# Kernel tuning notes

Measured on AMD Instinct MI355X. Metric: run time of the kernel, lower is better.

## Reference

```python
import jax, jax.numpy as jnp
import numpy as np

N_POI = 50000
D = 128
E = 400000
GCN_NUM = 3
HEADS = 8
B = 64
L = 100
LEAKY_SLOPE = 0.01
NORM_EPS = 1e-12


def setup_inputs() -> dict:
    key = jax.random.key(0)
    ks = jax.random.split(key, 11)
    return {
        "embeds": jax.random.normal(ks[0], (N_POI, D), jnp.float32) * 0.1,
        "gcn_W": jax.random.normal(ks[1], (GCN_NUM, D, D), jnp.float32) * (1.0 / np.sqrt(D)),
        "gcn_b": jnp.zeros((GCN_NUM, D), jnp.float32),
        "in_proj_w": jax.random.normal(ks[2], (3 * D, D), jnp.float32) * (1.0 / np.sqrt(D)),
        "in_proj_b": jnp.zeros((3 * D,), jnp.float32),
        "out_proj_w": jax.random.normal(ks[3], (D, D), jnp.float32) * (1.0 / np.sqrt(D)),
        "out_proj_b": jnp.zeros((D,), jnp.float32),
        "dist_vec": jax.random.uniform(ks[4], (E,), jnp.float32),
        "dist_edges": jax.random.randint(ks[5], (2, E), 0, N_POI),
        "x_idx": jax.random.randint(ks[6], (B * L,), 0, N_POI),
        "poi_idx": jax.random.randint(ks[7], (B,), 0, N_POI),
    }


def _self_attn(x, in_w, in_b, out_w, out_b):
    # x: [B, L, D]; standard nn.MultiheadAttention with Q=K=V=x, batch_first
    b, l, d = x.shape
    hd = d // HEADS
    qkv = x @ in_w.T + in_b                      # [B, L, 3D]
    q, k, v = jnp.split(qkv, 3, axis=-1)
    def heads(t):
        return t.reshape(b, l, HEADS, hd).transpose(0, 2, 1, 3)  # [B, H, L, hd]
    q, k, v = heads(q), heads(k), heads(v)
    scores = jnp.einsum('bhqd,bhkd->bhqk', q, k) / jnp.sqrt(jnp.asarray(hd, x.dtype))
    attn = jax.nn.softmax(scores, axis=-1)
    o = jnp.einsum('bhqk,bhkd->bhqd', attn, v).transpose(0, 2, 1, 3).reshape(b, l, d)
    return o @ out_w.T + out_b


def reference(embeds, gcn_W, gcn_b, in_proj_w, in_proj_b, out_proj_w, out_proj_b,
              dist_vec, dist_edges, x_idx, poi_idx):
    n_poi = embeds.shape[0]
    loop = jnp.arange(n_poi)
    # symmetrize edges + add self-loops (done in GeoGraph.__init__)
    rows = jnp.concatenate([dist_edges[0], dist_edges[1], loop])
    cols = jnp.concatenate([dist_edges[1], dist_edges[0], loop])
    dv = jnp.concatenate([dist_vec, dist_vec, jnp.zeros((n_poi,), dist_vec.dtype)])
    # symmetric degree normalization over destination (col) index
    deg = jax.ops.segment_sum(jnp.ones_like(dv), cols, num_segments=n_poi)
    dis = jnp.where(deg > 0, jax.lax.rsqrt(jnp.maximum(deg, 1e-12)), 0.0)
    w = jnp.exp(-dv ** 2) * dis[rows] * dis[cols]   # [E_full]

    enc = embeds
    for i in range(GCN_NUM):
        # sparse.mm: out[row] += w * enc[col]
        agg = jax.ops.segment_sum(w[:, None] * enc[cols], rows, num_segments=n_poi)
        enc = agg @ gcn_W[i].T + gcn_b[i]
        enc = jax.nn.leaky_relu(enc, LEAKY_SLOPE)
        enc = enc / jnp.maximum(jnp.linalg.norm(enc, axis=-1, keepdims=True), NORM_EPS)

    tar_embed = enc[poi_idx]                         # [B, D]
    geo_feat = enc[x_idx].reshape(B, L, D)           # equal-length sessions -> pad is a reshape
    attn_out = _self_attn(geo_feat, in_proj_w, in_proj_b, out_proj_w, out_proj_b)
    aggr_feat = attn_out.mean(axis=1)                # [B, D]
    return aggr_feat, tar_embed
```

## Files before the change

kernel.cpp:

```cpp
#include <hip/hip_runtime.h>
#include <math.h>

#define D 128
#define GCN_NUM 3
#define HEADS 8
#define HD 16
#define L_SEQ 100
#define LEAKY 0.01f
#define SC_BUCKETS 8

typedef __attribute__((ext_vector_type(8))) short short8v;
typedef __attribute__((ext_vector_type(4))) float f32x4;

__device__ __forceinline__ unsigned f2bf(float x) {
  unsigned u = __float_as_uint(x);
  return (u + 0x7FFFu + ((u >> 16) & 1u)) >> 16;
}
__device__ __forceinline__ float bflo2f(unsigned u) { return __uint_as_float(u << 16); }
__device__ __forceinline__ float bfhi2f(unsigned u) { return __uint_as_float(u & 0xFFFF0000u); }


__global__ void prep(const float* __restrict__ s0, unsigned short* __restrict__ d0, int n0,
                     const float* __restrict__ s1, unsigned short* __restrict__ d1, int n1,
                     const float* __restrict__ s2, unsigned short* __restrict__ d2, int n2,
                     int* __restrict__ deg, int N) {
  int i = blockIdx.x * blockDim.x + threadIdx.x;
  int n4tot = n0 + n1 + n2;
  if (i < n4tot) {
    const float* s; unsigned short* d; int j;
    if (i < n0)           { s = s0; d = d0; j = i; }
    else if (i < n0 + n1) { s = s1; d = d1; j = i - n0; }
    else                  { s = s2; d = d2; j = i - n0 - n1; }
    float4 v = reinterpret_cast<const float4*>(s)[j];
    uint2 o;
    o.x = f2bf(v.x) | (f2bf(v.y) << 16);
    o.y = f2bf(v.z) | (f2bf(v.w) << 16);
    reinterpret_cast<uint2*>(d)[j] = o;
  } else if (i - n4tot < N) {
    deg[i - n4tot] = 1;
  }
}


__global__ void count_deg(const int* __restrict__ e0, const int* __restrict__ e1,
                          int* __restrict__ deg, int E) {
  int stride = gridDim.x * blockDim.x;
  for (int i = blockIdx.x * blockDim.x + threadIdx.x; i < E; i += stride) {
    atomicAdd(&deg[e0[i]], 1);
    atomicAdd(&deg[e1[i]], 1);
  }
}


__global__ __launch_bounds__(1024) void block_sum(const int* __restrict__ deg,
                                                  int* __restrict__ bsum, int n) {
  __shared__ int ws[16];
  int tid = threadIdx.x, lane = tid & 63, wid = tid >> 6;
  int i = blockIdx.x * 1024 + tid;
  int v = (i < n) ? deg[i] : 0;
#pragma unroll
  for (int off = 32; off; off >>= 1) v += __shfl_xor(v, off);
  if (lane == 0) ws[wid] = v;
  __syncthreads();
  if (tid == 0) {
    int s = 0;
#pragma unroll
    for (int k = 0; k < 16; ++k) s += ws[k];
    bsum[blockIdx.x] = s;
  }
}

__global__ __launch_bounds__(1024) void scan_final(
    const int* __restrict__ deg, const int* __restrict__ bsum,
    int* __restrict__ row_ptr, int* __restrict__ cursor, int n, int nb) {
  __shared__ int ws[16];
  __shared__ int prefix_s;
  int tid = threadIdx.x, lane = tid & 63, wid = tid >> 6;
  int i = blockIdx.x * 1024 + tid;
  int v = (i < n) ? deg[i] : 0;
  int x = v;
#pragma unroll
  for (int off = 1; off < 64; off <<= 1) {
    int y = __shfl_up(x, off);
    if (lane >= off) x += y;
  }
  if (lane == 63) ws[wid] = x;
  __syncthreads();
  if (wid == 0) {
    int pv = (lane < blockIdx.x) ? bsum[lane] : 0;
#pragma unroll
    for (int off = 32; off; off >>= 1) pv += __shfl_xor(pv, off);
    if (lane == 0) prefix_s = pv;
    int s = (lane < 16) ? ws[lane] : 0;
#pragma unroll
    for (int off = 1; off < 16; off <<= 1) {
      int y = __shfl_up(s, off);
      if (lane >= off) s += y;
    }
    if (lane < 16) ws[lane] = s;
  }
  __syncthreads();
  int woff = wid ? ws[wid - 1] : 0;
  int prefix = prefix_s;
  if (i < n) {
    int pval = prefix + woff + (x - v);
    row_ptr[i] = pval;
    cursor[i] = pval;
  }
  if (blockIdx.x == nb - 1 && tid == 0) row_ptr[n] = prefix + ws[15];
}

__global__ __launch_bounds__(256) void scatter_edges_x(
    const int* __restrict__ e0, const int* __restrict__ e1,
    const float* __restrict__ dv, const int* __restrict__ deg,
    int* __restrict__ cursor, uint2* __restrict__ ecw,
    int E, int N, int span, int bpb) {
  int bucket = blockIdx.x & (SC_BUCKETS - 1);
  int bx = blockIdx.x >> 3;
  int rlo = bucket * span;
  int rhi = min(rlo + span, N);
  int total = 2 * E + N;
  int stride = bpb * 256;
  for (int i = bx * 256 + threadIdx.x; i < total; i += stride) {
    int r, c; bool self = false;
    if (i < E)          { r = e0[i];     c = e1[i]; }
    else if (i < 2 * E) { r = e1[i - E]; c = e0[i - E]; }
    else                { r = i - 2 * E; c = r; self = true; }
    if (r < rlo || r >= rhi) continue;
    float d = self ? 0.f : dv[(i < E) ? i : i - E];
    float w = expf(-d * d) * (1.0f / sqrtf((float)deg[r])) * (1.0f / sqrtf((float)deg[c]));
    int pos = atomicAdd(&cursor[r], 1);
    ecw[pos] = make_uint2((unsigned)c, __float_as_uint(w));
  }
}


__global__ __launch_bounds__(256) void spmm_bf(
    const int* __restrict__ row_ptr, const uint2* __restrict__ ecw,
    const unsigned short* __restrict__ enc, unsigned short* __restrict__ agg, int n) {
  int r = blockIdx.x * 4 + (threadIdx.x >> 6);
  if (r >= n) return;
  int lane = threadIdx.x & 63;
  int g = lane >> 4, t = lane & 15;
  int s = row_ptr[r], e = row_ptr[r + 1];
  float a0 = 0.f, a1 = 0.f, a2 = 0.f, a3 = 0.f, a4 = 0.f, a5 = 0.f, a6 = 0.f, a7 = 0.f;
  int i = s + g;
  uint2 cwA = make_uint2(0u, 0u), cwB = make_uint2(0u, 0u);
  if (i < e) cwA = ecw[i];
  if (i + 4 < e) cwB = ecw[i + 4];
  while (i + 4 < e) {
    uint2 cwC = cwA, cwD = cwB;
    if (i + 8 < e)  cwC = ecw[i + 8];
    if (i + 12 < e) cwD = ecw[i + 12];
    float wA = __uint_as_float(cwA.y), wB = __uint_as_float(cwB.y);
    uint4 uA = *reinterpret_cast<const uint4*>(enc + (size_t)cwA.x * D + t * 8);
    uint4 uB = *reinterpret_cast<const uint4*>(enc + (size_t)cwB.x * D + t * 8);
    a0 = fmaf(wA, bflo2f(uA.x), a0); a1 = fmaf(wA, bfhi2f(uA.x), a1);
    a2 = fmaf(wA, bflo2f(uA.y), a2); a3 = fmaf(wA, bfhi2f(uA.y), a3);
    a4 = fmaf(wA, bflo2f(uA.z), a4); a5 = fmaf(wA, bfhi2f(uA.z), a5);
    a6 = fmaf(wA, bflo2f(uA.w), a6); a7 = fmaf(wA, bfhi2f(uA.w), a7);
    a0 = fmaf(wB, bflo2f(uB.x), a0); a1 = fmaf(wB, bfhi2f(uB.x), a1);
    a2 = fmaf(wB, bflo2f(uB.y), a2); a3 = fmaf(wB, bfhi2f(uB.y), a3);
    a4 = fmaf(wB, bflo2f(uB.z), a4); a5 = fmaf(wB, bfhi2f(uB.z), a5);
    a6 = fmaf(wB, bflo2f(uB.w), a6); a7 = fmaf(wB, bfhi2f(uB.w), a7);
    cwA = cwC; cwB = cwD;
    i += 8;
  }
  if (i < e) {
    float wA = __uint_as_float(cwA.y);
    uint4 uA = *reinterpret_cast<const uint4*>(enc + (size_t)cwA.x * D + t * 8);
    a0 = fmaf(wA, bflo2f(uA.x), a0); a1 = fmaf(wA, bfhi2f(uA.x), a1);
    a2 = fmaf(wA, bflo2f(uA.y), a2); a3 = fmaf(wA, bfhi2f(uA.y), a3);
    a4 = fmaf(wA, bflo2f(uA.z), a4); a5 = fmaf(wA, bfhi2f(uA.z), a5);
    a6 = fmaf(wA, bflo2f(uA.w), a6); a7 = fmaf(wA, bfhi2f(uA.w), a7);
  }
  a0 += __shfl_xor(a0, 16); a0 += __shfl_xor(a0, 32);
  a1 += __shfl_xor(a1, 16); a1 += __shfl_xor(a1, 32);
  a2 += __shfl_xor(a2, 16); a2 += __shfl_xor(a2, 32);
  a3 += __shfl_xor(a3, 16); a3 += __shfl_xor(a3, 32);
  a4 += __shfl_xor(a4, 16); a4 += __shfl_xor(a4, 32);
  a5 += __shfl_xor(a5, 16); a5 += __shfl_xor(a5, 32);
  a6 += __shfl_xor(a6, 16); a6 += __shfl_xor(a6, 32);
  a7 += __shfl_xor(a7, 16); a7 += __shfl_xor(a7, 32);
  if (g == 0) {
    uint4 o;
    o.x = f2bf(a0) | (f2bf(a1) << 16);
    o.y = f2bf(a2) | (f2bf(a3) << 16);
    o.z = f2bf(a4) | (f2bf(a5) << 16);
    o.w = f2bf(a6) | (f2bf(a7) << 16);
    *reinterpret_cast<uint4*>(agg + (size_t)r * D + t * 8) = o;
  }
}

__global__ __launch_bounds__(256) void dense_mfma(
    const unsigned short* __restrict__ A, const unsigned short* __restrict__ Wb,
    const float* __restrict__ bias, unsigned short* __restrict__ enc, int n) {
  __shared__ unsigned short Wl[128 * 136];
  int tid = threadIdx.x;
  {
    int cg = (tid & 15) * 8;
    int r0 = tid >> 4;
#pragma unroll
    for (int i = 0; i < 8; ++i) {
      int row = r0 + i * 16;
      *reinterpret_cast<short8v*>(&Wl[row * 136 + cg]) =
          *reinterpret_cast<const short8v*>(Wb + row * D + cg);
    }
  }
  __syncthreads();
  int w = tid >> 6, lane = tid & 63;
  int lr = lane & 15, lg = lane >> 4;
#pragma unroll
  for (int rt = 0; rt < 2; ++rt) {
    int rbase = blockIdx.x * 128 + rt * 64 + w * 16;
    f32x4 acc[8];
#pragma unroll
    for (int j = 0; j < 8; ++j) acc[j] = f32x4{0.f, 0.f, 0.f, 0.f};
    const unsigned short* arow = A + (size_t)(rbase + lr) * D + lg * 8;
#pragma unroll
    for (int ks = 0; ks < 4; ++ks) {
      short8v a = *reinterpret_cast<const short8v*>(arow + ks * 32);
#pragma unroll
      for (int jt = 0; jt < 8; ++jt) {
        short8v b = *reinterpret_cast<const short8v*>(&Wl[(jt * 16 + lr) * 136 + ks * 32 + lg * 8]);
        acc[jt] = __builtin_amdgcn_mfma_f32_16x16x32_bf16(a, b, acc[jt], 0, 0, 0);
      }
    }
    float vals[8][4];
    float ss[4] = {0.f, 0.f, 0.f, 0.f};
#pragma unroll
    for (int jt = 0; jt < 8; ++jt) {
      float bj = bias[jt * 16 + lr];
#pragma unroll
      for (int i = 0; i < 4; ++i) {
        float t = acc[jt][i] + bj;
        t = (t > 0.f) ? t : LEAKY * t;
        vals[jt][i] = t;
        ss[i] += t * t;
      }
    }
#pragma unroll
    for (int i = 0; i < 4; ++i) {
      float s = ss[i];
      s += __shfl_xor(s, 1); s += __shfl_xor(s, 2);
      s += __shfl_xor(s, 4); s += __shfl_xor(s, 8);
      ss[i] = 1.0f / fmaxf(sqrtf(s), 1e-12f);
    }
#pragma unroll
    for (int i = 0; i < 4; ++i) {
      int row = rbase + lg * 4 + i;
      if (row < n) {
#pragma unroll
        for (int jt = 0; jt < 8; ++jt)
          enc[(size_t)row * D + jt * 16 + lr] = (unsigned short)f2bf(vals[jt][i] * ss[i]);
      }
    }
  }
}


__global__ void gather_tar(const unsigned short* __restrict__ src,
                           const int* __restrict__ poi_idx, float* __restrict__ tar, int B) {
  int j = blockIdx.x;
  if (j < B) {
    int t = threadIdx.x;
    unsigned u = reinterpret_cast<const unsigned*>(src + (size_t)poi_idx[j] * D)[t];
    reinterpret_cast<float2*>(tar + (size_t)j * D)[t] = make_float2(bflo2f(u), bfhi2f(u));
  }
}

__global__ __launch_bounds__(256) void qkv_mfma(
    const unsigned short* __restrict__ enc, const int* __restrict__ x_idx,
    const unsigned short* __restrict__ Wb, const float* __restrict__ bias,
    float* __restrict__ qkv, int M) {
  __shared__ unsigned short Wl[128 * 136];
  int tid = threadIdx.x;
  const unsigned short* Wslab = Wb + (size_t)blockIdx.y * 128 * D;
  {
    int cg = (tid & 15) * 8;
    int r0 = tid >> 4;
#pragma unroll
    for (int i = 0; i < 8; ++i) {
      int row = r0 + i * 16;
      *reinterpret_cast<short8v*>(&Wl[row * 136 + cg]) =
          *reinterpret_cast<const short8v*>(Wslab + row * D + cg);
    }
  }
  __syncthreads();
  int w = tid >> 6, lane = tid & 63;
  int lr = lane & 15, lg = lane >> 4;
  int colbase = blockIdx.y * 128;
#pragma unroll
  for (int rt = 0; rt < 2; ++rt) {
    int rbase = blockIdx.x * 128 + rt * 64 + w * 16;
    f32x4 acc[8];
#pragma unroll
    for (int j = 0; j < 8; ++j) acc[j] = f32x4{0.f, 0.f, 0.f, 0.f};
    const unsigned short* arow = enc + (size_t)x_idx[rbase + lr] * D + lg * 8;
#pragma unroll
    for (int ks = 0; ks < 4; ++ks) {
      short8v a = *reinterpret_cast<const short8v*>(arow + ks * 32);
#pragma unroll
      for (int jt = 0; jt < 8; ++jt) {
        short8v b = *reinterpret_cast<const short8v*>(&Wl[(jt * 16 + lr) * 136 + ks * 32 + lg * 8]);
        acc[jt] = __builtin_amdgcn_mfma_f32_16x16x32_bf16(a, b, acc[jt], 0, 0, 0);
      }
    }
#pragma unroll
    for (int jt = 0; jt < 8; ++jt) {
      int j = colbase + jt * 16 + lr;
      float bj = bias[j];
#pragma unroll
      for (int i = 0; i < 4; ++i) {
        int row = rbase + lg * 4 + i;
        if (row < M) qkv[(size_t)row * 384 + j] = acc[jt][i] + bj;
      }
    }
  }
}

__global__ __launch_bounds__(128) void attn_kernel(
    const float* __restrict__ qkv, float* __restrict__ o) {
  __shared__ float k_s[L_SEQ][HD];
  __shared__ float v_s[L_SEQ][HD];
  __shared__ float sc[L_SEQ][L_SEQ + 1];
  int b = blockIdx.x / HEADS;
  int h = blockIdx.x % HEADS;
  int tid = threadIdx.x;
  const size_t rowbase = (size_t)b * L_SEQ;
  for (int idx = tid; idx < L_SEQ * HD; idx += 128) {
    int l = idx >> 4, d2 = idx & 15;
    const float* base = qkv + (rowbase + l) * 384 + h * HD + d2;
    k_s[l][d2] = base[128];
    v_s[l][d2] = base[256];
  }
  __syncthreads();
  if (tid < L_SEQ) {
    float q[HD];
    const float* qp = qkv + (rowbase + tid) * 384 + h * HD;
#pragma unroll
    for (int d2 = 0; d2 < HD; ++d2) q[d2] = qp[d2];
    float m = -1e30f;
    for (int j = 0; j < L_SEQ; ++j) {
      float s = 0.f;
#pragma unroll
      for (int d2 = 0; d2 < HD; ++d2) s += q[d2] * k_s[j][d2];
      s *= 0.25f;
      sc[tid][j] = s;
      m = fmaxf(m, s);
    }
    float sum = 0.f;
    for (int j = 0; j < L_SEQ; ++j) {
      float e = expf(sc[tid][j] - m);
      sc[tid][j] = e;
      sum += e;
    }
    float inv = 1.f / sum;
    float oacc[HD];
#pragma unroll
    for (int d2 = 0; d2 < HD; ++d2) oacc[d2] = 0.f;
    for (int j = 0; j < L_SEQ; ++j) {
      float p = sc[tid][j];
#pragma unroll
      for (int d2 = 0; d2 < HD; ++d2) oacc[d2] += p * v_s[j][d2];
    }
    float* op = o + (rowbase + tid) * D + h * HD;
#pragma unroll
    for (int d2 = 0; d2 < HD; ++d2) op[d2] = oacc[d2] * inv;
  }
}

__global__ __launch_bounds__(128) void out_mean_kernel(
    const float* __restrict__ o, const float* __restrict__ Wo,
    const float* __restrict__ bo, float* __restrict__ out, int L) {
  __shared__ float m_s[D];
  int b = blockIdx.x, tid = threadIdx.x;
  float s = 0.f;
  for (int l = 0; l < L; ++l) s += o[((size_t)b * L + l) * D + tid];
  m_s[tid] = s / (float)L;
  __syncthreads();
  const float4* w4 = reinterpret_cast<const float4*>(Wo + (size_t)tid * D);
  float acc = 0.f;
  for (int k4 = 0; k4 < D / 4; ++k4) {
    float4 w = w4[k4];
    int k = k4 * 4;
    acc += m_s[k] * w.x + m_s[k + 1] * w.y + m_s[k + 2] * w.z + m_s[k + 3] * w.w;
  }
  out[(size_t)b * D + tid] = acc + bo[tid];
}


extern "C" void kernel_launch(void* const* d_in, const int* in_sizes, int n_in,
                              void* d_out, int out_size, void* d_ws, size_t ws_size,
                              hipStream_t stream) {
  const float* embeds   = (const float*)d_in[0];
  const float* gcn_W    = (const float*)d_in[1];
  const float* gcn_b    = (const float*)d_in[2];
  const float* in_w     = (const float*)d_in[3];
  const float* in_b     = (const float*)d_in[4];
  const float* out_w    = (const float*)d_in[5];
  const float* out_b    = (const float*)d_in[6];
  const float* dist_vec = (const float*)d_in[7];
  const int*   edges    = (const int*)d_in[8];
  const int*   x_idx    = (const int*)d_in[9];
  const int*   poi_idx  = (const int*)d_in[10];
  float* out = (float*)d_out;

  int N  = in_sizes[0] / D;
  int E  = in_sizes[7];
  int BL = in_sizes[9];
  int B  = in_sizes[10];
  int L  = BL / B;
  const int* e0 = edges;
  const int* e1 = edges + E;
  size_t total_edges = (size_t)2 * E + N;
  int Npad = ((N + 127) / 128) * 128;
  int NB   = (N + 1023) / 1024;

  char* p = (char*)d_ws;
  auto alloc = [&](size_t bytes) { char* q = p; p += (bytes + 255) & ~(size_t)255; return q; };
  int*   deg     = (int*)alloc((size_t)N * 4);
  int*   row_ptr = (int*)alloc((size_t)(N + 1) * 4);
  int*   cursor  = (int*)alloc((size_t)N * 4);
  int*   bsum    = (int*)alloc((size_t)NB * 4);
  uint2* ecw     = (uint2*)alloc(total_edges * 8);
  unsigned short* emb_bf = (unsigned short*)alloc((size_t)Npad * D * 2);
  unsigned short* W_bf   = (unsigned short*)alloc((size_t)GCN_NUM * D * D * 2);
  unsigned short* inw_bf = (unsigned short*)alloc((size_t)3 * D * D * 2);
  unsigned short* agg_bf = (unsigned short*)alloc((size_t)Npad * D * 2);
  unsigned short* enc_bf = (unsigned short*)alloc((size_t)Npad * D * 2);
  float* qkv  = (float*)alloc((size_t)BL * 384 * 4);
  float* obuf = (float*)alloc((size_t)BL * D * 4);

  int n4e = N * D / 4, n4w = GCN_NUM * D * D / 4, n4i = 3 * D * D / 4;
  int prep_tot = n4e + n4w + n4i + N;
  prep<<<(prep_tot + 255) / 256, 256, 0, stream>>>(
      embeds, emb_bf, n4e, gcn_W, W_bf, n4w, in_w, inw_bf, n4i, deg, N);

  count_deg<<<1024, 256, 0, stream>>>(e0, e1, deg, E);
  block_sum<<<NB, 1024, 0, stream>>>(deg, bsum, N);
  scan_final<<<NB, 1024, 0, stream>>>(deg, bsum, row_ptr, cursor, N, NB);
  int span = (N + SC_BUCKETS - 1) / SC_BUCKETS;
  int bpb = 512;
  scatter_edges_x<<<SC_BUCKETS * bpb, 256, 0, stream>>>(
      e0, e1, dist_vec, deg, cursor, ecw, E, N, span, bpb);

  const unsigned short* cur_in = emb_bf;
  for (int i = 0; i < GCN_NUM; ++i) {
    spmm_bf<<<(N + 3) / 4, 256, 0, stream>>>(row_ptr, ecw, cur_in, agg_bf, N);
    dense_mfma<<<Npad / 128, 256, 0, stream>>>(
        agg_bf, W_bf + (size_t)i * D * D, gcn_b + (size_t)i * D, enc_bf, N);
    cur_in = enc_bf;
  }

  gather_tar<<<B, 64, 0, stream>>>(enc_bf, poi_idx, out + (size_t)B * D, B);
  dim3 qgrid(BL / 128, 3);
  qkv_mfma<<<qgrid, 256, 0, stream>>>(enc_bf, x_idx, inw_bf, in_b, qkv, BL);
  attn_kernel<<<B * HEADS, 128, 0, stream>>>(qkv, obuf);
  out_mean_kernel<<<B, 128, 0, stream>>>(obuf, out_w, out_b, out, L);
}
```

Baseline: 364.4 us.

## Bucket edge scatter by hardware XCC id with per-bucket dynamic chunk queue

The edge scatter kernel now reads the hardware XCC id and assigns each block to the row bucket of the chiplet it runs on. Blocks then pull edge chunks from a per-bucket atomic work counter, which prep resets to zero. The aim is to keep each bucket's cursor atomics and ecw writes local to one XCC's L2 and to balance work dynamically. It assumes blocks are spread over all 8 XCCs; if any XCC runs no blocks, that bucket's edges are never written. It also adds a global atomic and two barriers per chunk.

```diff
diff --git a/kernel.cpp b/kernel.cpp
--- a/kernel.cpp
+++ b/kernel.cpp
@@ -8,6 +8,7 @@
 #define L_SEQ 100
 #define LEAKY 0.01f
 #define SC_BUCKETS 8
+#define SC_CHUNK 2048
 
 typedef __attribute__((ext_vector_type(8))) short short8v;
 typedef __attribute__((ext_vector_type(4))) float f32x4;
@@ -23,7 +24,7 @@
 __global__ void prep(const float* __restrict__ s0, unsigned short* __restrict__ d0, int n0,
                      const float* __restrict__ s1, unsigned short* __restrict__ d1, int n1,
                      const float* __restrict__ s2, unsigned short* __restrict__ d2, int n2,
-                     int* __restrict__ deg, int N) {
+                     int* __restrict__ deg, int N, int* __restrict__ chunk_ctr) {
   int i = blockIdx.x * blockDim.x + threadIdx.x;
   int n4tot = n0 + n1 + n2;
   if (i < n4tot) {
@@ -39,6 +40,7 @@
   } else if (i - n4tot < N) {
     deg[i - n4tot] = 1;
   }
+  if (i < SC_BUCKETS) chunk_ctr[i] = 0;
 }
 
 
@@ -110,27 +112,38 @@
   if (blockIdx.x == nb - 1 && tid == 0) row_ptr[n] = prefix + ws[15];
 }
 
-__global__ __launch_bounds__(256) void scatter_edges_x(
+__global__ __launch_bounds__(256) void scatter_edges_xcc(
     const int* __restrict__ e0, const int* __restrict__ e1,
     const float* __restrict__ dv, const int* __restrict__ deg,
-    int* __restrict__ cursor, uint2* __restrict__ ecw,
-    int E, int N, int span, int bpb) {
-  int bucket = blockIdx.x & (SC_BUCKETS - 1);
-  int bx = blockIdx.x >> 3;
+    int* __restrict__ cursor, int* __restrict__ chunk_ctr, uint2* __restrict__ ecw,
+    int E, int N, int span) {
+  unsigned xcc;
+  asm volatile("s_getreg_b32 %0, hwreg(HW_REG_XCC_ID)" : "=s"(xcc));
+  int bucket = (int)(xcc & (SC_BUCKETS - 1));
   int rlo = bucket * span;
   int rhi = min(rlo + span, N);
   int total = 2 * E + N;
-  int stride = bpb * 256;
-  for (int i = bx * 256 + threadIdx.x; i < total; i += stride) {
-    int r, c; bool self = false;
-    if (i < E)          { r = e0[i];     c = e1[i]; }
-    else if (i < 2 * E) { r = e1[i - E]; c = e0[i - E]; }
-    else                { r = i - 2 * E; c = r; self = true; }
-    if (r < rlo || r >= rhi) continue;
-    float d = self ? 0.f : dv[(i < E) ? i : i - E];
-    float w = expf(-d * d) * (1.0f / sqrtf((float)deg[r])) * (1.0f / sqrtf((float)deg[c]));
-    int pos = atomicAdd(&cursor[r], 1);
-    ecw[pos] = make_uint2((unsigned)c, __float_as_uint(w));
+  int nchunks = (total + SC_CHUNK - 1) / SC_CHUNK;
+  __shared__ int chunk_s;
+  for (;;) {
+    __syncthreads();
+    if (threadIdx.x == 0) chunk_s = atomicAdd(&chunk_ctr[bucket], 1);
+    __syncthreads();
+    int ch = chunk_s;
+    if (ch >= nchunks) break;
+    int base = ch * SC_CHUNK;
+    int end = min(base + SC_CHUNK, total);
+    for (int i = base + (int)threadIdx.x; i < end; i += 256) {
+      int r, c; bool self = false;
+      if (i < E)          { r = e0[i];     c = e1[i]; }
+      else if (i < 2 * E) { r = e1[i - E]; c = e0[i - E]; }
+      else                { r = i - 2 * E; c = r; self = true; }
+      if (r < rlo || r >= rhi) continue;
+      float d = self ? 0.f : dv[(i < E) ? i : i - E];
+      float w = expf(-d * d) * (1.0f / sqrtf((float)deg[r])) * (1.0f / sqrtf((float)deg[c]));
+      int pos = atomicAdd(&cursor[r], 1);
+      ecw[pos] = make_uint2((unsigned)c, __float_as_uint(w));
+    }
   }
 }
 
@@ -419,11 +432,12 @@
 
   char* p = (char*)d_ws;
   auto alloc = [&](size_t bytes) { char* q = p; p += (bytes + 255) & ~(size_t)255; return q; };
-  int*   deg     = (int*)alloc((size_t)N * 4);
-  int*   row_ptr = (int*)alloc((size_t)(N + 1) * 4);
-  int*   cursor  = (int*)alloc((size_t)N * 4);
-  int*   bsum    = (int*)alloc((size_t)NB * 4);
-  uint2* ecw     = (uint2*)alloc(total_edges * 8);
+  int*   deg       = (int*)alloc((size_t)N * 4);
+  int*   row_ptr   = (int*)alloc((size_t)(N + 1) * 4);
+  int*   cursor    = (int*)alloc((size_t)N * 4);
+  int*   bsum      = (int*)alloc((size_t)NB * 4);
+  int*   chunk_ctr = (int*)alloc((size_t)SC_BUCKETS * 4);
+  uint2* ecw       = (uint2*)alloc(total_edges * 8);
   unsigned short* emb_bf = (unsigned short*)alloc((size_t)Npad * D * 2);
   unsigned short* W_bf   = (unsigned short*)alloc((size_t)GCN_NUM * D * D * 2);
   unsigned short* inw_bf = (unsigned short*)alloc((size_t)3 * D * D * 2);
@@ -435,15 +449,14 @@
   int n4e = N * D / 4, n4w = GCN_NUM * D * D / 4, n4i = 3 * D * D / 4;
   int prep_tot = n4e + n4w + n4i + N;
   prep<<<(prep_tot + 255) / 256, 256, 0, stream>>>(
-      embeds, emb_bf, n4e, gcn_W, W_bf, n4w, in_w, inw_bf, n4i, deg, N);
+      embeds, emb_bf, n4e, gcn_W, W_bf, n4w, in_w, inw_bf, n4i, deg, N, chunk_ctr);
 
   count_deg<<<1024, 256, 0, stream>>>(e0, e1, deg, E);
   block_sum<<<NB, 1024, 0, stream>>>(deg, bsum, N);
   scan_final<<<NB, 1024, 0, stream>>>(deg, bsum, row_ptr, cursor, N, NB);
   int span = (N + SC_BUCKETS - 1) / SC_BUCKETS;
-  int bpb = 512;
-  scatter_edges_x<<<SC_BUCKETS * bpb, 256, 0, stream>>>(
-      e0, e1, dist_vec, deg, cursor, ecw, E, N, span, bpb);
+  scatter_edges_xcc<<<2048, 256, 0, stream>>>(
+      e0, e1, dist_vec, deg, cursor, chunk_ctr, ecw, E, N, span);
 
   const unsigned short* cur_in = emb_bf;
   for (int i = 0; i < GCN_NUM; ++i) {
```

After: 408.7 us. 1.12x slower.

## Slice features per XCD and pack edges into 32-bit col/bf16 weight

Applied to the files above, without the earlier changes.

Stores node embeddings in 8 feature slices of 16 columns each. The new SpMM reads the hardware XCC id so that each XCD processes only one slice, keeping that slice's gather working set inside its own L2. Row chunks are handed out dynamically through per-slice atomic counters, which are reset in the prep kernel. Each edge is packed into 32 bits (16-bit column index plus bf16 weight), halving edge traffic. The catches are that node counts must stay below 65536, edge weights lose precision, and the dense and gather kernels must read and write the strided slice layout.

```diff
diff --git a/kernel.cpp b/kernel.cpp
--- a/kernel.cpp
+++ b/kernel.cpp
@@ -23,14 +23,22 @@
 __global__ void prep(const float* __restrict__ s0, unsigned short* __restrict__ d0, int n0,
                      const float* __restrict__ s1, unsigned short* __restrict__ d1, int n1,
                      const float* __restrict__ s2, unsigned short* __restrict__ d2, int n2,
-                     int* __restrict__ deg, int N) {
+                     int* __restrict__ deg, int N, int* __restrict__ ctr, size_t strideS) {
   int i = blockIdx.x * blockDim.x + threadIdx.x;
   int n4tot = n0 + n1 + n2;
-  if (i < n4tot) {
+  if (i < n0) {
+    float4 v = reinterpret_cast<const float4*>(s0)[i];
+    int row = i >> 5;
+    int k = (i & 31) * 4;
+    uint2 o;
+    o.x = f2bf(v.x) | (f2bf(v.y) << 16);
+    o.y = f2bf(v.z) | (f2bf(v.w) << 16);
+    unsigned short* dst = d0 + (size_t)(k >> 4) * strideS + (size_t)row * 16 + (k & 15);
+    *reinterpret_cast<uint2*>(dst) = o;
+  } else if (i < n4tot) {
     const float* s; unsigned short* d; int j;
-    if (i < n0)           { s = s0; d = d0; j = i; }
-    else if (i < n0 + n1) { s = s1; d = d1; j = i - n0; }
-    else                  { s = s2; d = d2; j = i - n0 - n1; }
+    if (i < n0 + n1) { s = s1; d = d1; j = i - n0; }
+    else             { s = s2; d = d2; j = i - n0 - n1; }
     float4 v = reinterpret_cast<const float4*>(s)[j];
     uint2 o;
     o.x = f2bf(v.x) | (f2bf(v.y) << 16);
@@ -39,6 +47,7 @@
   } else if (i - n4tot < N) {
     deg[i - n4tot] = 1;
   }
+  if (i < GCN_NUM * 8) ctr[i] = 0;
 }
 
 
@@ -50,7 +59,6 @@
     atomicAdd(&deg[e1[i]], 1);
   }
 }
-
 
 __global__ __launch_bounds__(1024) void block_sum(const int* __restrict__ deg,
                                                   int* __restrict__ bsum, int n) {
@@ -110,10 +118,10 @@
   if (blockIdx.x == nb - 1 && tid == 0) row_ptr[n] = prefix + ws[15];
 }
 
-__global__ __launch_bounds__(256) void scatter_edges_x(
+__global__ __launch_bounds__(256) void scatter_edges_p(
     const int* __restrict__ e0, const int* __restrict__ e1,
     const float* __restrict__ dv, const int* __restrict__ deg,
-    int* __restrict__ cursor, uint2* __restrict__ ecw,
+    int* __restrict__ cursor, unsigned* __restrict__ ecw,
     int E, int N, int span, int bpb) {
   int bucket = blockIdx.x & (SC_BUCKETS - 1);
   int bx = blockIdx.x >> 3;
@@ -130,71 +138,64 @@
     float d = self ? 0.f : dv[(i < E) ? i : i - E];
     float w = expf(-d * d) * (1.0f / sqrtf((float)deg[r])) * (1.0f / sqrtf((float)deg[c]));
     int pos = atomicAdd(&cursor[r], 1);
-    ecw[pos] = make_uint2((unsigned)c, __float_as_uint(w));
-  }
-}
-
-
-__global__ __launch_bounds__(256) void spmm_bf(
-    const int* __restrict__ row_ptr, const uint2* __restrict__ ecw,
-    const unsigned short* __restrict__ enc, unsigned short* __restrict__ agg, int n) {
-  int r = blockIdx.x * 4 + (threadIdx.x >> 6);
-  if (r >= n) return;
-  int lane = threadIdx.x & 63;
-  int g = lane >> 4, t = lane & 15;
-  int s = row_ptr[r], e = row_ptr[r + 1];
-  float a0 = 0.f, a1 = 0.f, a2 = 0.f, a3 = 0.f, a4 = 0.f, a5 = 0.f, a6 = 0.f, a7 = 0.f;
-  int i = s + g;
-  uint2 cwA = make_uint2(0u, 0u), cwB = make_uint2(0u, 0u);
-  if (i < e) cwA = ecw[i];
-  if (i + 4 < e) cwB = ecw[i + 4];
-  while (i + 4 < e) {
-    uint2 cwC = cwA, cwD = cwB;
-    if (i + 8 < e)  cwC = ecw[i + 8];
-    if (i + 12 < e) cwD = ecw[i + 12];
-    float wA = __uint_as_float(cwA.y), wB = __uint_as_float(cwB.y);
-    uint4 uA = *reinterpret_cast<const uint4*>(enc + (size_t)cwA.x * D + t * 8);
-    uint4 uB = *reinterpret_cast<const uint4*>(enc + (size_t)cwB.x * D + t * 8);
-    a0 = fmaf(wA, bflo2f(uA.x), a0); a1 = fmaf(wA, bfhi2f(uA.x), a1);
-    a2 = fmaf(wA, bflo2f(uA.y), a2); a3 = fmaf(wA, bfhi2f(uA.y), a3);
-    a4 = fmaf(wA, bflo2f(uA.z), a4); a5 = fmaf(wA, bfhi2f(uA.z), a5);
-    a6 = fmaf(wA, bflo2f(uA.w), a6); a7 = fmaf(wA, bfhi2f(uA.w), a7);
-    a0 = fmaf(wB, bflo2f(uB.x), a0); a1 = fmaf(wB, bfhi2f(uB.x), a1);
-    a2 = fmaf(wB, bflo2f(uB.y), a2); a3 = fmaf(wB, bfhi2f(uB.y), a3);
-    a4 = fmaf(wB, bflo2f(uB.z), a4); a5 = fmaf(wB, bfhi2f(uB.z), a5);
-    a6 = fmaf(wB, bflo2f(uB.w), a6); a7 = fmaf(wB, bfhi2f(uB.w), a7);
-    cwA = cwC; cwB = cwD;
-    i += 8;
-  }
-  if (i < e) {
-    float wA = __uint_as_float(cwA.y);
-    uint4 uA = *reinterpret_cast<const uint4*>(enc + (size_t)cwA.x * D + t * 8);
-    a0 = fmaf(wA, bflo2f(uA.x), a0); a1 = fmaf(wA, bfhi2f(uA.x), a1);
-    a2 = fmaf(wA, bflo2f(uA.y), a2); a3 = fmaf(wA, bfhi2f(uA.y), a3);
-    a4 = fmaf(wA, bflo2f(uA.z), a4); a5 = fmaf(wA, bfhi2f(uA.z), a5);
-    a6 = fmaf(wA, bflo2f(uA.w), a6); a7 = fmaf(wA, bfhi2f(uA.w), a7);
-  }
-  a0 += __shfl_xor(a0, 16); a0 += __shfl_xor(a0, 32);
-  a1 += __shfl_xor(a1, 16); a1 += __shfl_xor(a1, 32);
-  a2 += __shfl_xor(a2, 16); a2 += __shfl_xor(a2, 32);
-  a3 += __shfl_xor(a3, 16); a3 += __shfl_xor(a3, 32);
-  a4 += __shfl_xor(a4, 16); a4 += __shfl_xor(a4, 32);
-  a5 += __shfl_xor(a5, 16); a5 += __shfl_xor(a5, 32);
-  a6 += __shfl_xor(a6, 16); a6 += __shfl_xor(a6, 32);
-  a7 += __shfl_xor(a7, 16); a7 += __shfl_xor(a7, 32);
-  if (g == 0) {
-    uint4 o;
-    o.x = f2bf(a0) | (f2bf(a1) << 16);
-    o.y = f2bf(a2) | (f2bf(a3) << 16);
-    o.z = f2bf(a4) | (f2bf(a5) << 16);
-    o.w = f2bf(a6) | (f2bf(a7) << 16);
-    *reinterpret_cast<uint4*>(agg + (size_t)r * D + t * 8) = o;
+    ecw[pos] = (unsigned)c | (f2bf(w) << 16);
+  }
+}
+
+
+__global__ __launch_bounds__(256) void spmm_slice(
+    const int* __restrict__ row_ptr, const unsigned* __restrict__ ecw,
+    const unsigned short* __restrict__ in_s, unsigned short* __restrict__ out_s,
+    int* __restrict__ ctr, int n, size_t strideS) {
+  unsigned xcc;
+  asm volatile("s_getreg_b32 %0, hwreg(HW_REG_XCC_ID)" : "=s"(xcc));
+  int slice = (int)(xcc & 7u);
+  const unsigned short* in = in_s + (size_t)slice * strideS;
+  unsigned short* out = out_s + (size_t)slice * strideS;
+  int tid = threadIdx.x;
+  int grp = tid >> 4;
+  int sub = (tid >> 3) & 1;
+  int fl = tid & 7;
+  int nch = (n + 63) >> 6;
+  __shared__ int chunk_s;
+  for (;;) {
+    __syncthreads();
+    if (tid == 0) chunk_s = atomicAdd(&ctr[slice], 1);
+    __syncthreads();
+    int ch = chunk_s;
+    if (ch >= nch) break;
+    int rbase = ch << 6;
+#pragma unroll
+    for (int ps = 0; ps < 4; ++ps) {
+      int r = rbase + ps * 16 + grp;
+      if (r >= n) continue;
+      int sE = row_ptr[r], eE = row_ptr[r + 1];
+      float acc0 = 0.f, acc1 = 0.f;
+      int i = sE + sub;
+      unsigned dA = (i < eE) ? ecw[i] : 0u;
+      unsigned dB = (i + 2 < eE) ? ecw[i + 2] : 0u;
+      while (i < eE) {
+        unsigned dn = (i + 4 < eE) ? ecw[i + 4] : 0u;
+        float w = bfhi2f(dA);
+        unsigned u = *reinterpret_cast<const unsigned*>(in + (size_t)(dA & 0xFFFFu) * 16 + fl * 2);
+        acc0 = fmaf(w, bflo2f(u), acc0);
+        acc1 = fmaf(w, bfhi2f(u), acc1);
+        dA = dB; dB = dn; i += 2;
+      }
+      acc0 += __shfl_xor(acc0, 8);
+      acc1 += __shfl_xor(acc1, 8);
+      if (sub == 0) {
+        unsigned o = f2bf(acc0) | (f2bf(acc1) << 16);
+        *reinterpret_cast<unsigned*>(out + (size_t)r * 16 + fl * 2) = o;
+      }
+    }
   }
 }
 
 __global__ __launch_bounds__(256) void dense_mfma(
     const unsigned short* __restrict__ A, const unsigned short* __restrict__ Wb,
-    const float* __restrict__ bias, unsigned short* __restrict__ enc, int n) {
+    const float* __restrict__ bias, unsigned short* __restrict__ enc,
+    int n, size_t strideS) {
   __shared__ unsigned short Wl[128 * 136];
   int tid = threadIdx.x;
   {
@@ -216,10 +217,10 @@
     f32x4 acc[8];
 #pragma unroll
     for (int j = 0; j < 8; ++j) acc[j] = f32x4{0.f, 0.f, 0.f, 0.f};
-    const unsigned short* arow = A + (size_t)(rbase + lr) * D + lg * 8;
+    const unsigned short* abase = A + (size_t)(rbase + lr) * 16 + (lg & 1) * 8;
 #pragma unroll
     for (int ks = 0; ks < 4; ++ks) {
-      short8v a = *reinterpret_cast<const short8v*>(arow + ks * 32);
+      short8v a = *reinterpret_cast<const short8v*>(abase + (size_t)(2 * ks + (lg >> 1)) * strideS);
 #pragma unroll
       for (int jt = 0; jt < 8; ++jt) {
         short8v b = *reinterpret_cast<const short8v*>(&Wl[(jt * 16 + lr) * 136 + ks * 32 + lg * 8]);
@@ -252,7 +253,8 @@
       if (row < n) {
 #pragma unroll
         for (int jt = 0; jt < 8; ++jt)
-          enc[(size_t)row * D + jt * 16 + lr] = (unsigned short)f2bf(vals[jt][i] * ss[i]);
+          enc[(size_t)jt * strideS + (size_t)row * 16 + lr] =
+              (unsigned short)f2bf(vals[jt][i] * ss[i]);
       }
     }
   }
@@ -260,11 +262,15 @@
 
 
 __global__ void gather_tar(const unsigned short* __restrict__ src,
-                           const int* __restrict__ poi_idx, float* __restrict__ tar, int B) {
+                           const int* __restrict__ poi_idx, float* __restrict__ tar,
+                           int B, size_t strideS) {
   int j = blockIdx.x;
   if (j < B) {
     int t = threadIdx.x;
-    unsigned u = reinterpret_cast<const unsigned*>(src + (size_t)poi_idx[j] * D)[t];
+    int f = t * 2;
+    size_t idx = (size_t)poi_idx[j];
+    unsigned u = *reinterpret_cast<const unsigned*>(
+        src + (size_t)(f >> 4) * strideS + idx * 16 + (f & 15));
     reinterpret_cast<float2*>(tar + (size_t)j * D)[t] = make_float2(bflo2f(u), bfhi2f(u));
   }
 }
@@ -272,7 +278,7 @@
 __global__ __launch_bounds__(256) void qkv_mfma(
     const unsigned short* __restrict__ enc, const int* __restrict__ x_idx,
     const unsigned short* __restrict__ Wb, const float* __restrict__ bias,
-    float* __restrict__ qkv, int M) {
+    float* __restrict__ qkv, int M, size_t strideS) {
   __shared__ unsigned short Wl[128 * 136];
   int tid = threadIdx.x;
   const unsigned short* Wslab = Wb + (size_t)blockIdx.y * 128 * D;
@@ -296,10 +302,11 @@
     f32x4 acc[8];
 #pragma unroll
     for (int j = 0; j < 8; ++j) acc[j] = f32x4{0.f, 0.f, 0.f, 0.f};
-    const unsigned short* arow = enc + (size_t)x_idx[rbase + lr] * D + lg * 8;
+    const unsigned short* abase =
+        enc + (size_t)x_idx[rbase + lr] * 16 + (lg & 1) * 8;
 #pragma unroll
     for (int ks = 0; ks < 4; ++ks) {
-      short8v a = *reinterpret_cast<const short8v*>(arow + ks * 32);
+      short8v a = *reinterpret_cast<const short8v*>(abase + (size_t)(2 * ks + (lg >> 1)) * strideS);
 #pragma unroll
       for (int jt = 0; jt < 8; ++jt) {
         short8v b = *reinterpret_cast<const short8v*>(&Wl[(jt * 16 + lr) * 136 + ks * 32 + lg * 8]);
@@ -416,14 +423,16 @@
   size_t total_edges = (size_t)2 * E + N;
   int Npad = ((N + 127) / 128) * 128;
   int NB   = (N + 1023) / 1024;
+  size_t strideS = (size_t)Npad * 16;
 
   char* p = (char*)d_ws;
   auto alloc = [&](size_t bytes) { char* q = p; p += (bytes + 255) & ~(size_t)255; return q; };
-  int*   deg     = (int*)alloc((size_t)N * 4);
-  int*   row_ptr = (int*)alloc((size_t)(N + 1) * 4);
-  int*   cursor  = (int*)alloc((size_t)N * 4);
-  int*   bsum    = (int*)alloc((size_t)NB * 4);
-  uint2* ecw     = (uint2*)alloc(total_edges * 8);
+  int*      deg      = (int*)alloc((size_t)N * 4);
+  int*      row_ptr  = (int*)alloc((size_t)(N + 1) * 4);
+  int*      cursor   = (int*)alloc((size_t)N * 4);
+  int*      bsum     = (int*)alloc((size_t)NB * 4);
+  int*      spmm_ctr = (int*)alloc((size_t)GCN_NUM * 8 * 4);
+  unsigned* ecw      = (unsigned*)alloc(total_edges * 4);
   unsigned short* emb_bf = (unsigned short*)alloc((size_t)Npad * D * 2);
   unsigned short* W_bf   = (unsigned short*)alloc((size_t)GCN_NUM * D * D * 2);
   unsigned short* inw_bf = (unsigned short*)alloc((size_t)3 * D * D * 2);
@@ -435,27 +444,28 @@
   int n4e = N * D / 4, n4w = GCN_NUM * D * D / 4, n4i = 3 * D * D / 4;
   int prep_tot = n4e + n4w + n4i + N;
   prep<<<(prep_tot + 255) / 256, 256, 0, stream>>>(
-      embeds, emb_bf, n4e, gcn_W, W_bf, n4w, in_w, inw_bf, n4i, deg, N);
+      embeds, emb_bf, n4e, gcn_W, W_bf, n4w, in_w, inw_bf, n4i, deg, N, spmm_ctr, strideS);
 
   count_deg<<<1024, 256, 0, stream>>>(e0, e1, deg, E);
   block_sum<<<NB, 1024, 0, stream>>>(deg, bsum, N);
   scan_final<<<NB, 1024, 0, stream>>>(deg, bsum, row_ptr, cursor, N, NB);
   int span = (N + SC_BUCKETS - 1) / SC_BUCKETS;
   int bpb = 512;
-  scatter_edges_x<<<SC_BUCKETS * bpb, 256, 0, stream>>>(
+  scatter_edges_p<<<SC_BUCKETS * bpb, 256, 0, stream>>>(
       e0, e1, dist_vec, deg, cursor, ecw, E, N, span, bpb);
 
   const unsigned short* cur_in = emb_bf;
   for (int i = 0; i < GCN_NUM; ++i) {
-    spmm_bf<<<(N + 3) / 4, 256, 0, stream>>>(row_ptr, ecw, cur_in, agg_bf, N);
+    spmm_slice<<<2048, 256, 0, stream>>>(row_ptr, ecw, cur_in, agg_bf,
+                                         spmm_ctr + i * 8, N, strideS);
     dense_mfma<<<Npad / 128, 256, 0, stream>>>(
-        agg_bf, W_bf + (size_t)i * D * D, gcn_b + (size_t)i * D, enc_bf, N);
+        agg_bf, W_bf + (size_t)i * D * D, gcn_b + (size_t)i * D, enc_bf, N, strideS);
     cur_in = enc_bf;
   }
 
-  gather_tar<<<B, 64, 0, stream>>>(enc_bf, poi_idx, out + (size_t)B * D, B);
+  gather_tar<<<B, 64, 0, stream>>>(enc_bf, poi_idx, out + (size_t)B * D, B, strideS);
   dim3 qgrid(BL / 128, 3);
-  qkv_mfma<<<qgrid, 256, 0, stream>>>(enc_bf, x_idx, inw_bf, in_b, qkv, BL);
+  qkv_mfma<<<qgrid, 256, 0, stream>>>(enc_bf, x_idx, inw_bf, in_b, qkv, BL, strideS);
   attn_kernel<<<B * HEADS, 128, 0, stream>>>(qkv, obuf);
   out_mean_kernel<<<B, 128, 0, stream>>>(obuf, out_w, out_b, out, L);
 }
```

Measured after the change: 613.1 us. 1.68x slower.
